# Kernel tuning notes

Hardware: AMD Instinct MI355X
Metric: run time of the kernel (lower is better)

The kernel has to match this reference:

```python
import jax, jax.numpy as jnp
import numpy as np

B, S, D = 4, 2048, 1024
NH, HD = 16, 64  # num_heads, head_dim; NH*HD == D


def setup_inputs() -> dict:
    key = jax.random.key(0)
    ks = jax.random.split(key, 10)
    s = 0.02
    return {
        "x": jax.random.normal(ks[0], (B, S, D), dtype=jnp.float32),
        "attention_mask": jnp.zeros((B, 1, 1, S), dtype=jnp.float32),
        "Wq": jax.random.normal(ks[1], (D, D), dtype=jnp.float32) * s,
        "bq": jnp.zeros((D,), dtype=jnp.float32),
        "Wk": jax.random.normal(ks[2], (D, D), dtype=jnp.float32) * s,
        "bk": jnp.zeros((D,), dtype=jnp.float32),
        "Wv": jax.random.normal(ks[3], (D, D), dtype=jnp.float32) * s,
        "bv": jnp.zeros((D,), dtype=jnp.float32),
        "Wo": jax.random.normal(ks[4], (D, D), dtype=jnp.float32) * s,
        "bo": jnp.zeros((D,), dtype=jnp.float32),
    }


def _heads(t):
    # [B,S,D] -> [B,NH,S,HD]
    return t.reshape(B, S, NH, HD).transpose(0, 2, 1, 3)


def reference(x, attention_mask, Wq, bq, Wk, bk, Wv, bv, Wo, bo):
    q = _heads(x @ Wq + bq)
    k = _heads(x @ Wk + bk)
    v = _heads(x @ Wv + bv)
    scores = jnp.einsum("bhqd,bhkd->bhqk", q, k) / jnp.sqrt(jnp.float32(HD))
    scores = scores + attention_mask
    attn = jax.nn.softmax(scores, axis=-1)  # dropout p=0 -> identity
    ctx = jnp.einsum("bhqk,bhkd->bhqd", attn, v)
    ctx = ctx.transpose(0, 2, 1, 3).reshape(B, S, D)
    return ctx @ Wo + bo
```

## Files before the change

kernel.cpp:

```cpp
#include <hip/hip_runtime.h>
#include <cstdint>
#include <cstddef>

typedef unsigned short u16;
typedef __attribute__((ext_vector_type(8))) __bf16 bf16x8;
typedef __attribute__((ext_vector_type(4))) float f32x4;
typedef __attribute__((ext_vector_type(16))) float f32x16;
typedef __attribute__((ext_vector_type(2))) uint32_t u32x2;
typedef __attribute__((ext_vector_type(4))) float float4v;

#define BATCH 4
#define S_LEN 2048
#define DMODEL 1024
#define NHEAD 16
#define HDIM 64
#define MROWS (BATCH * S_LEN)
#define LOG2E 1.4426950408889634f
#define SC_L (0.125f * LOG2E)

__device__ __forceinline__ u16 f2bf(float f) {
  uint32_t u = __float_as_uint(f);
  u += 0x7fffu + ((u >> 16) & 1u);
  return (u16)(u >> 16);
}

#if __has_builtin(__builtin_amdgcn_cvt_pk_bf16_f32)
__device__ __forceinline__ uint32_t packbf2(float a, float b) {
  auto t = __builtin_amdgcn_cvt_pk_bf16_f32(a, b);
  uint32_t u;
  __builtin_memcpy(&u, &t, 4);
  return u;
}
#else
__device__ __forceinline__ uint32_t packbf2(float a, float b) {
  uint32_t ua = __float_as_uint(a) + 0x8000u;
  uint32_t ub = __float_as_uint(b) + 0x8000u;
  return (ub & 0xFFFF0000u) | (ua >> 16);
}
#endif

#if __has_builtin(__builtin_amdgcn_exp2f)
#define EXP2(x) __builtin_amdgcn_exp2f(x)
#else
#define EXP2(x) exp2f(x)
#endif

typedef __attribute__((address_space(1))) void gvoid_t;
typedef __attribute__((address_space(3))) void svoid_t;
__device__ __forceinline__ void gl_lds16(const void* g, void* s) {
  __builtin_amdgcn_global_load_lds((gvoid_t*)g, (svoid_t*)s, 16, 0, 0);
}

#define NB_CVT (MROWS * DMODEL / 4 / 256)
#define NB_W   4096
__global__ __launch_bounds__(256) void prep_kernel(const float4v* __restrict__ x,
                                                   u32x2* __restrict__ xb,
                                                   const float* __restrict__ W0,
                                                   const float* __restrict__ W1,
                                                   const float* __restrict__ W2,
                                                   const float* __restrict__ W3,
                                                   u16* __restrict__ Wall,
                                                   const float* __restrict__ mask,
                                                   float* __restrict__ mL) {
  __shared__ float tile[32][33];
  const int bid = blockIdx.x;
  const int tid = threadIdx.x;
  if (bid < NB_CVT) {
    const int i = bid * 256 + tid;
    float4v v = x[i];
    u32x2 o;
    o.x = packbf2(v.x, v.y);
    o.y = packbf2(v.z, v.w);
    xb[i] = o;
    return;
  }
  if (bid >= NB_CVT + NB_W) {
    const int i = (bid - NB_CVT - NB_W) * 256 + tid;
    mL[i] = mask[i] * LOG2E;
    return;
  }
  const int r = bid - NB_CVT;
  const int z = r >> 10;
  const int rem = r & 1023;
  const float* W = (z == 0) ? W0 : (z == 1) ? W1 : (z == 2) ? W2 : W3;
  u16* Wt = Wall + (size_t)z * DMODEL * DMODEL;
  const int n0 = (rem & 31) * 32, k0 = (rem >> 5) * 32;
  const int xx = tid & 31, y = tid >> 5;
  for (int yy = y; yy < 32; yy += 8)
    tile[yy][xx] = W[(size_t)(k0 + yy) * DMODEL + n0 + xx];
  __syncthreads();
  for (int yy = y; yy < 32; yy += 8)
    Wt[(size_t)(n0 + yy) * DMODEL + k0 + xx] = f2bf(tile[xx][yy]);
}

template <int MODE>
__global__ __launch_bounds__(256) void gemm128(const u16* __restrict__ A,
                                               const u16* __restrict__ Bt,
                                               const float* __restrict__ b0,
                                               const float* __restrict__ b1,
                                               const float* __restrict__ b2,
                                               void* __restrict__ o0,
                                               void* __restrict__ o1,
                                               void* __restrict__ o2) {
  __shared__ u16 As[2 * 128 * 32];
  __shared__ u16 Bs[2 * 128 * 32];
  const int tid = threadIdx.x;
  const int wid = tid >> 6;
  const int lane = tid & 63;
  const int l16 = lane & 15;
  const int g4 = lane >> 4;
  const int m0 = blockIdx.x * 128;
  const int n0 = blockIdx.y * 128;
  const int wm = (wid & 1) * 64;
  const int wn = (wid >> 1) * 64;

  const int srow = tid >> 2;
  const int sk = (tid & 3) * 8;
  const u16* gA = A + (size_t)(m0 + srow) * DMODEL + sk;
  const u16* gB = Bt + (size_t)(n0 + srow) * DMODEL + sk;
  char* sA = (char*)As + wid * 1024;
  char* sB = (char*)Bs + wid * 1024;

  f32x4 acc[4][4];
#pragma unroll
  for (int i = 0; i < 4; ++i)
#pragma unroll
    for (int j = 0; j < 4; ++j) acc[i][j] = (f32x4){0.f, 0.f, 0.f, 0.f};

  for (int k0 = 0; k0 < DMODEL; k0 += 64) {
    __syncthreads();
    gl_lds16(gA + k0, sA);
    gl_lds16(gA + (size_t)64 * DMODEL + k0, sA + 4096);
    gl_lds16(gB + k0, sB);
    gl_lds16(gB + (size_t)64 * DMODEL + k0, sB + 4096);
    gl_lds16(gA + k0 + 32, sA + 8192);
    gl_lds16(gA + (size_t)64 * DMODEL + k0 + 32, sA + 12288);
    gl_lds16(gB + k0 + 32, sB + 8192);
    gl_lds16(gB + (size_t)64 * DMODEL + k0 + 32, sB + 12288);
    __syncthreads();

#pragma unroll
    for (int kk = 0; kk < 2; ++kk) {
      const u16* Ab = As + kk * 4096;
      const u16* Bb = Bs + kk * 4096;
      bf16x8 af[4], bfr[4];
#pragma unroll
      for (int i = 0; i < 4; ++i)
        af[i] = *(const bf16x8*)(Ab + (wm + i * 16 + l16) * 32 + g4 * 8);
#pragma unroll
      for (int j = 0; j < 4; ++j)
        bfr[j] = *(const bf16x8*)(Bb + (wn + j * 16 + l16) * 32 + g4 * 8);
#pragma unroll
      for (int i = 0; i < 4; ++i)
#pragma unroll
        for (int j = 0; j < 4; ++j)
          acc[i][j] = __builtin_amdgcn_mfma_f32_16x16x32_bf16(af[i], bfr[j],
                                                              acc[i][j], 0, 0, 0);
    }
  }

  const int seg = n0 >> 10;
  const float* bp = (MODE == 1 || seg == 0) ? b0 : (seg == 1 ? b1 : b2);
  void* op = (MODE == 1 || seg == 0) ? o0 : (seg == 1 ? o1 : o2);

#pragma unroll
  for (int i = 0; i < 4; ++i) {
#pragma unroll
    for (int j = 0; j < 4; ++j) {
      const int coll = n0 + wn + j * 16 + l16;
      const int cseg = coll & 1023;
      const float bval = bp[cseg];
#pragma unroll
      for (int r = 0; r < 4; ++r) {
        const int rowg = m0 + wm + i * 16 + g4 * 4 + r;
        const float v = acc[i][j][r] + bval;
        if (MODE == 0) {
          const int b = rowg >> 11, s = rowg & (S_LEN - 1);
          const int h = cseg >> 6, d = cseg & (HDIM - 1);
          if (seg == 2) {
            ((u16*)op)[(((size_t)(b * NHEAD + h) * HDIM + d) << 11) + s] = f2bf(v);
          } else {
            ((u16*)op)[((size_t)((b * NHEAD + h) * S_LEN + s) << 6) + d] = f2bf(v);
          }
        } else {
          ((float*)op)[(size_t)rowg * DMODEL + cseg] = v;
        }
      }
    }
  }
}

__global__ __launch_bounds__(256, 2) void attn8_kernel(const u16* __restrict__ Q,
                                                       const u16* __restrict__ K,
                                                       const u16* __restrict__ Vt,
                                                       const float* __restrict__ maskL,
                                                       u16* __restrict__ ctx) {
  __shared__ u16 Ks[64 * 72];
  __shared__ u16 Vs[64 * 72];

  const int tid = threadIdx.x;
  const int wid = tid >> 6;
  const int lane = tid & 63;
  const int l32 = lane & 31;
  const int hi = lane >> 5;
  const int flat = blockIdx.y * gridDim.x + blockIdx.x;
  const int nf = (flat & 7) * 64 + (flat >> 3);
  const int bx = nf & 7;
  const int bh = nf >> 3;
  const int b = bh >> 4;
  const int h = bh & 15;
  const int qw0 = bx * 256 + wid * 64;

  const u16* Qbase = Q + (size_t)bh * S_LEN * HDIM;
  bf16x8 aq[2][4];
#pragma unroll
  for (int qh = 0; qh < 2; ++qh)
#pragma unroll
    for (int c = 0; c < 4; ++c)
      aq[qh][c] = *(const bf16x8*)(Qbase + (size_t)(qw0 + qh * 32 + l32) * HDIM +
                                   c * 16 + hi * 8);

  const f32x16 z16 = {};
  f32x16 oacc[2][2] = {};
  float lsum[2] = {0.f, 0.f};

  const int srow = tid >> 3;
  const int scol = (tid & 7) * 8;
  const int keyg = scol >> 4;
  const int todd = (scol >> 3) & 1;
  const int vkb = keyg * 16 + todd * 4;
  const u16* Kg = K + (size_t)bh * S_LEN * HDIM + (size_t)srow * HDIM + scol;
  const u16* Vg = Vt + (size_t)bh * HDIM * S_LEN + (size_t)srow * S_LEN + scol;
  const float* mrow = maskL + (size_t)b * S_LEN;

  for (int kt = 0; kt < S_LEN; kt += 64) {
    bf16x8 kv0 = *(const bf16x8*)(Kg + (size_t)kt * HDIM);
    bf16x8 kv1 = *(const bf16x8*)(Kg + (size_t)(kt + 32) * HDIM);
    union { bf16x8 v; uint32_t u[4]; } vv0, vv1;
    vv0.v = *(const bf16x8*)(Vg + kt);
    vv1.v = *(const bf16x8*)(Vg + (size_t)32 * S_LEN + kt);
    __syncthreads();
    *(bf16x8*)(Ks + srow * 72 + scol) = kv0;
    *(bf16x8*)(Ks + (srow + 32) * 72 + scol) = kv1;
    *(u32x2*)(Vs + srow * 72 + vkb) = (u32x2){vv0.u[0], vv0.u[1]};
    *(u32x2*)(Vs + srow * 72 + vkb + 8) = (u32x2){vv0.u[2], vv0.u[3]};
    *(u32x2*)(Vs + (srow + 32) * 72 + vkb) = (u32x2){vv1.u[0], vv1.u[1]};
    *(u32x2*)(Vs + (srow + 32) * 72 + vkb + 8) = (u32x2){vv1.u[2], vv1.u[3]};
    __syncthreads();

    uint32_t P[2][2][8];
#pragma unroll
    for (int T = 0; T < 2; ++T) {
      bf16x8 kf[4];
#pragma unroll
      for (int c = 0; c < 4; ++c)
        kf[c] = *(const bf16x8*)(Ks + (T * 32 + l32) * 72 + c * 16 + hi * 8);
      f32x4 m4[4];
#pragma unroll
      for (int tq = 0; tq < 4; ++tq)
        m4[tq] = *(const f32x4*)(mrow + kt + T * 32 + tq * 8 + hi * 4);
#pragma unroll
      for (int qh = 0; qh < 2; ++qh) {
        f32x16 s = __builtin_amdgcn_mfma_f32_32x32x16_bf16(kf[0], aq[qh][0], z16, 0, 0, 0);
#pragma unroll
        for (int c = 1; c < 4; ++c)
          s = __builtin_amdgcn_mfma_f32_32x32x16_bf16(kf[c], aq[qh][c], s, 0, 0, 0);
        float lacc_t = 0.f;
#pragma unroll
        for (int tq = 0; tq < 4; ++tq) {
          float p0 = EXP2(fmaf(s[tq * 4 + 0], SC_L, m4[tq][0]));
          float p1 = EXP2(fmaf(s[tq * 4 + 1], SC_L, m4[tq][1]));
          float p2 = EXP2(fmaf(s[tq * 4 + 2], SC_L, m4[tq][2]));
          float p3 = EXP2(fmaf(s[tq * 4 + 3], SC_L, m4[tq][3]));
          P[T][qh][tq * 2] = packbf2(p0, p1);
          P[T][qh][tq * 2 + 1] = packbf2(p2, p3);
          lacc_t += (p0 + p1) + (p2 + p3);
        }
        lsum[qh] += lacc_t;
      }
    }

#pragma unroll
    for (int c = 0; c < 4; ++c) {
      const int T = c >> 1, half = c & 1;
      bf16x8 vf[2];
#pragma unroll
      for (int dh = 0; dh < 2; ++dh)
        vf[dh] = *(const bf16x8*)(Vs + (dh * 32 + l32) * 72 + c * 16 + hi * 8);
#pragma unroll
      for (int qh = 0; qh < 2; ++qh) {
        union { uint32_t u[4]; bf16x8 v; } pf;
#pragma unroll
        for (int e = 0; e < 4; ++e) pf.u[e] = P[T][qh][half * 4 + e];
        oacc[qh][0] = __builtin_amdgcn_mfma_f32_32x32x16_bf16(pf.v, vf[0], oacc[qh][0], 0, 0, 0);
        oacc[qh][1] = __builtin_amdgcn_mfma_f32_32x32x16_bf16(pf.v, vf[1], oacc[qh][1], 0, 0, 0);
      }
    }
  }

  float lt[2];
#pragma unroll
  for (int qh = 0; qh < 2; ++qh)
    lt[qh] = lsum[qh] + __shfl_xor(lsum[qh], 32);

#pragma unroll
  for (int qh = 0; qh < 2; ++qh) {
#pragma unroll
    for (int reg = 0; reg < 16; ++reg) {
      const int qloc = (reg & 3) + 8 * (reg >> 2) + 4 * hi;
      const int q = qw0 + qh * 32 + qloc;
      const float inv = 1.0f / __shfl(lt[qh], qloc);
      u16* cp = ctx + ((size_t)(b * S_LEN + q) * NHEAD + h) * HDIM;
      cp[l32] = f2bf(oacc[qh][0][reg] * inv);
      cp[32 + l32] = f2bf(oacc[qh][1][reg] * inv);
    }
  }
}

extern "C" void kernel_launch(void* const* d_in, const int* in_sizes, int n_in,
                              void* d_out, int out_size, void* d_ws, size_t ws_size,
                              hipStream_t stream) {
  const float* x = (const float*)d_in[0];
  const float* mask = (const float*)d_in[1];
  const float* Wq = (const float*)d_in[2];
  const float* bq = (const float*)d_in[3];
  const float* Wk = (const float*)d_in[4];
  const float* bk = (const float*)d_in[5];
  const float* Wv = (const float*)d_in[6];
  const float* bv = (const float*)d_in[7];
  const float* Wo = (const float*)d_in[8];
  const float* bo = (const float*)d_in[9];
  float* out = (float*)d_out;

  char* ws = (char*)d_ws;
  size_t off = 0;
  u16* xb = (u16*)(ws + off);    off += (size_t)MROWS * DMODEL * 2;
  u16* wall = (u16*)(ws + off);  off += (size_t)4 * DMODEL * DMODEL * 2;
  u16* Qh = (u16*)(ws + off);    off += (size_t)MROWS * DMODEL * 2;
  u16* Kh = (u16*)(ws + off);    off += (size_t)MROWS * DMODEL * 2;
  u16* Vtb = (u16*)(ws + off);   off += (size_t)MROWS * DMODEL * 2;
  u16* ctxb = (u16*)(ws + off);  off += (size_t)MROWS * DMODEL * 2;
  float* mL = (float*)(ws + off); off += (size_t)BATCH * S_LEN * 4;
  (void)ws_size; (void)in_sizes; (void)n_in; (void)out_size;

  prep_kernel<<<dim3(NB_CVT + NB_W + BATCH * S_LEN / 256), dim3(256), 0, stream>>>(
      (const float4v*)x, (u32x2*)xb, Wq, Wk, Wv, Wo, wall, mask, mL);

  gemm128<0><<<dim3(MROWS / 128, 3 * DMODEL / 128), dim3(256), 0, stream>>>(
      xb, wall, bq, bk, bv, (void*)Qh, (void*)Kh, (void*)Vtb);

  attn8_kernel<<<dim3(S_LEN / 256, BATCH * NHEAD), dim3(256), 0, stream>>>(Qh, Kh, Vtb, mL, ctxb);

  gemm128<1><<<dim3(MROWS / 128, DMODEL / 128), dim3(256), 0, stream>>>(
      ctxb, wall + (size_t)3 * DMODEL * DMODEL, bo, bo, bo, (void*)out, (void*)out, (void*)out);
}
```

Before: 289.4 us.

## Double attention key tile per barrier and compute row sums via MFMA with ones

The attention kernel now stages 128 keys per iteration instead of 64, so it does half as many syncthreads pairs and issues more global loads in flight. The softmax denominator is no longer summed with scalar adds and a cross-lane shuffle. It is accumulated by an extra MFMA of P against a ones vector, which leaves the sum already in the output register layout. This trades VALU adds and shuffles for extra matrix-core work (50% more PV MFMAs), plus higher LDS use and register pressure. The sum is now taken over the bf16-rounded P values.

```diff
diff --git a/kernel.cpp b/kernel.cpp
--- a/kernel.cpp
+++ b/kernel.cpp
@@ -190,13 +190,13 @@
   }
 }
 
-__global__ __launch_bounds__(256, 2) void attn8_kernel(const u16* __restrict__ Q,
+__global__ __launch_bounds__(256, 2) void attn9_kernel(const u16* __restrict__ Q,
                                                        const u16* __restrict__ K,
                                                        const u16* __restrict__ Vt,
                                                        const float* __restrict__ maskL,
                                                        u16* __restrict__ ctx) {
-  __shared__ u16 Ks[64 * 72];
-  __shared__ u16 Vs[64 * 72];
+  __shared__ u16 Ks[128 * 72];
+  __shared__ u16 Vs[64 * 136];
 
   const int tid = threadIdx.x;
   const int wid = tid >> 6;
@@ -220,9 +220,14 @@
       aq[qh][c] = *(const bf16x8*)(Qbase + (size_t)(qw0 + qh * 32 + l32) * HDIM +
                                    c * 16 + hi * 8);
 
+  union { u16 s[8]; bf16x8 v; } onesu;
+#pragma unroll
+  for (int i = 0; i < 8; ++i) onesu.s[i] = 0x3F80;
+  const bf16x8 onesv = onesu.v;
+
   const f32x16 z16 = {};
   f32x16 oacc[2][2] = {};
-  float lsum[2] = {0.f, 0.f};
+  f32x16 lacc[2] = {};
 
   const int srow = tid >> 3;
   const int scol = (tid & 7) * 8;
@@ -233,83 +238,92 @@
   const u16* Vg = Vt + (size_t)bh * HDIM * S_LEN + (size_t)srow * S_LEN + scol;
   const float* mrow = maskL + (size_t)b * S_LEN;
 
-  for (int kt = 0; kt < S_LEN; kt += 64) {
+  for (int kt = 0; kt < S_LEN; kt += 128) {
     bf16x8 kv0 = *(const bf16x8*)(Kg + (size_t)kt * HDIM);
     bf16x8 kv1 = *(const bf16x8*)(Kg + (size_t)(kt + 32) * HDIM);
-    union { bf16x8 v; uint32_t u[4]; } vv0, vv1;
+    bf16x8 kv2 = *(const bf16x8*)(Kg + (size_t)(kt + 64) * HDIM);
+    bf16x8 kv3 = *(const bf16x8*)(Kg + (size_t)(kt + 96) * HDIM);
+    union { bf16x8 v; uint32_t u[4]; } vv0, vv1, vv2, vv3;
     vv0.v = *(const bf16x8*)(Vg + kt);
     vv1.v = *(const bf16x8*)(Vg + (size_t)32 * S_LEN + kt);
+    vv2.v = *(const bf16x8*)(Vg + kt + 64);
+    vv3.v = *(const bf16x8*)(Vg + (size_t)32 * S_LEN + kt + 64);
     __syncthreads();
     *(bf16x8*)(Ks + srow * 72 + scol) = kv0;
     *(bf16x8*)(Ks + (srow + 32) * 72 + scol) = kv1;
-    *(u32x2*)(Vs + srow * 72 + vkb) = (u32x2){vv0.u[0], vv0.u[1]};
-    *(u32x2*)(Vs + srow * 72 + vkb + 8) = (u32x2){vv0.u[2], vv0.u[3]};
-    *(u32x2*)(Vs + (srow + 32) * 72 + vkb) = (u32x2){vv1.u[0], vv1.u[1]};
-    *(u32x2*)(Vs + (srow + 32) * 72 + vkb + 8) = (u32x2){vv1.u[2], vv1.u[3]};
+    *(bf16x8*)(Ks + (srow + 64) * 72 + scol) = kv2;
+    *(bf16x8*)(Ks + (srow + 96) * 72 + scol) = kv3;
+    *(u32x2*)(Vs + srow * 136 + vkb) = (u32x2){vv0.u[0], vv0.u[1]};
+    *(u32x2*)(Vs + srow * 136 + vkb + 8) = (u32x2){vv0.u[2], vv0.u[3]};
+    *(u32x2*)(Vs + (srow + 32) * 136 + vkb) = (u32x2){vv1.u[0], vv1.u[1]};
+    *(u32x2*)(Vs + (srow + 32) * 136 + vkb + 8) = (u32x2){vv1.u[2], vv1.u[3]};
+    *(u32x2*)(Vs + srow * 136 + 64 + vkb) = (u32x2){vv2.u[0], vv2.u[1]};
+    *(u32x2*)(Vs + srow * 136 + 64 + vkb + 8) = (u32x2){vv2.u[2], vv2.u[3]};
+    *(u32x2*)(Vs + (srow + 32) * 136 + 64 + vkb) = (u32x2){vv3.u[0], vv3.u[1]};
+    *(u32x2*)(Vs + (srow + 32) * 136 + 64 + vkb + 8) = (u32x2){vv3.u[2], vv3.u[3]};
     __syncthreads();
 
-    uint32_t P[2][2][8];
-#pragma unroll
-    for (int T = 0; T < 2; ++T) {
-      bf16x8 kf[4];
-#pragma unroll
-      for (int c = 0; c < 4; ++c)
-        kf[c] = *(const bf16x8*)(Ks + (T * 32 + l32) * 72 + c * 16 + hi * 8);
-      f32x4 m4[4];
-#pragma unroll
-      for (int tq = 0; tq < 4; ++tq)
-        m4[tq] = *(const f32x4*)(mrow + kt + T * 32 + tq * 8 + hi * 4);
-#pragma unroll
-      for (int qh = 0; qh < 2; ++qh) {
-        f32x16 s = __builtin_amdgcn_mfma_f32_32x32x16_bf16(kf[0], aq[qh][0], z16, 0, 0, 0);
-#pragma unroll
-        for (int c = 1; c < 4; ++c)
-          s = __builtin_amdgcn_mfma_f32_32x32x16_bf16(kf[c], aq[qh][c], s, 0, 0, 0);
-        float lacc_t = 0.f;
-#pragma unroll
-        for (int tq = 0; tq < 4; ++tq) {
-          float p0 = EXP2(fmaf(s[tq * 4 + 0], SC_L, m4[tq][0]));
-          float p1 = EXP2(fmaf(s[tq * 4 + 1], SC_L, m4[tq][1]));
-          float p2 = EXP2(fmaf(s[tq * 4 + 2], SC_L, m4[tq][2]));
-          float p3 = EXP2(fmaf(s[tq * 4 + 3], SC_L, m4[tq][3]));
-          P[T][qh][tq * 2] = packbf2(p0, p1);
-          P[T][qh][tq * 2 + 1] = packbf2(p2, p3);
-          lacc_t += (p0 + p1) + (p2 + p3);
+#pragma unroll
+    for (int ko = 0; ko < 128; ko += 64) {
+      const u16* Kb = Ks + ko * 72;
+      const u16* Vb = Vs + ko;
+      const float* mko = mrow + kt + ko;
+
+      uint32_t P[2][2][8];
+#pragma unroll
+      for (int T = 0; T < 2; ++T) {
+        bf16x8 kf[4];
+#pragma unroll
+        for (int c = 0; c < 4; ++c)
+          kf[c] = *(const bf16x8*)(Kb + (T * 32 + l32) * 72 + c * 16 + hi * 8);
+        f32x4 m4[4];
+#pragma unroll
+        for (int tq = 0; tq < 4; ++tq)
+          m4[tq] = *(const f32x4*)(mko + T * 32 + tq * 8 + hi * 4);
+#pragma unroll
+        for (int qh = 0; qh < 2; ++qh) {
+          f32x16 s = __builtin_amdgcn_mfma_f32_32x32x16_bf16(kf[0], aq[qh][0], z16, 0, 0, 0);
+#pragma unroll
+          for (int c = 1; c < 4; ++c)
+            s = __builtin_amdgcn_mfma_f32_32x32x16_bf16(kf[c], aq[qh][c], s, 0, 0, 0);
+#pragma unroll
+          for (int tq = 0; tq < 4; ++tq) {
+            float p0 = EXP2(fmaf(s[tq * 4 + 0], SC_L, m4[tq][0]));
+            float p1 = EXP2(fmaf(s[tq * 4 + 1], SC_L, m4[tq][1]));
+            float p2 = EXP2(fmaf(s[tq * 4 + 2], SC_L, m4[tq][2]));
+            float p3 = EXP2(fmaf(s[tq * 4 + 3], SC_L, m4[tq][3]));
+            P[T][qh][tq * 2] = packbf2(p0, p1);
+            P[T][qh][tq * 2 + 1] = packbf2(p2, p3);
+          }
         }
-        lsum[qh] += lacc_t;
+      }
+
+#pragma unroll
+      for (int c = 0; c < 4; ++c) {
+        const int T = c >> 1, half = c & 1;
+        bf16x8 vf[2];
+#pragma unroll
+        for (int dh = 0; dh < 2; ++dh)
+          vf[dh] = *(const bf16x8*)(Vb + (dh * 32 + l32) * 136 + c * 16 + hi * 8);
+#pragma unroll
+        for (int qh = 0; qh < 2; ++qh) {
+          union { uint32_t u[4]; bf16x8 v; } pf;
+#pragma unroll
+          for (int e = 0; e < 4; ++e) pf.u[e] = P[T][qh][half * 4 + e];
+          oacc[qh][0] = __builtin_amdgcn_mfma_f32_32x32x16_bf16(pf.v, vf[0], oacc[qh][0], 0, 0, 0);
+          oacc[qh][1] = __builtin_amdgcn_mfma_f32_32x32x16_bf16(pf.v, vf[1], oacc[qh][1], 0, 0, 0);
+          lacc[qh] = __builtin_amdgcn_mfma_f32_32x32x16_bf16(pf.v, onesv, lacc[qh], 0, 0, 0);
+        }
       }
     }
-
-#pragma unroll
-    for (int c = 0; c < 4; ++c) {
-      const int T = c >> 1, half = c & 1;
-      bf16x8 vf[2];
-#pragma unroll
-      for (int dh = 0; dh < 2; ++dh)
-        vf[dh] = *(const bf16x8*)(Vs + (dh * 32 + l32) * 72 + c * 16 + hi * 8);
-#pragma unroll
-      for (int qh = 0; qh < 2; ++qh) {
-        union { uint32_t u[4]; bf16x8 v; } pf;
-#pragma unroll
-        for (int e = 0; e < 4; ++e) pf.u[e] = P[T][qh][half * 4 + e];
-        oacc[qh][0] = __builtin_amdgcn_mfma_f32_32x32x16_bf16(pf.v, vf[0], oacc[qh][0], 0, 0, 0);
-        oacc[qh][1] = __builtin_amdgcn_mfma_f32_32x32x16_bf16(pf.v, vf[1], oacc[qh][1], 0, 0, 0);
-      }
-    }
-  }
-
-  float lt[2];
-#pragma unroll
-  for (int qh = 0; qh < 2; ++qh)
-    lt[qh] = lsum[qh] + __shfl_xor(lsum[qh], 32);
+  }
 
 #pragma unroll
   for (int qh = 0; qh < 2; ++qh) {
 #pragma unroll
     for (int reg = 0; reg < 16; ++reg) {
-      const int qloc = (reg & 3) + 8 * (reg >> 2) + 4 * hi;
-      const int q = qw0 + qh * 32 + qloc;
-      const float inv = 1.0f / __shfl(lt[qh], qloc);
+      const int q = qw0 + qh * 32 + (reg & 3) + 8 * (reg >> 2) + 4 * hi;
+      const float inv = 1.0f / lacc[qh][reg];
       u16* cp = ctx + ((size_t)(b * S_LEN + q) * NHEAD + h) * HDIM;
       cp[l32] = f2bf(oacc[qh][0][reg] * inv);
       cp[32 + l32] = f2bf(oacc[qh][1][reg] * inv);
@@ -349,7 +363,7 @@
   gemm128<0><<<dim3(MROWS / 128, 3 * DMODEL / 128), dim3(256), 0, stream>>>(
       xb, wall, bq, bk, bv, (void*)Qh, (void*)Kh, (void*)Vtb);
 
-  attn8_kernel<<<dim3(S_LEN / 256, BATCH * NHEAD), dim3(256), 0, stream>>>(Qh, Kh, Vtb, mL, ctxb);
+  attn9_kernel<<<dim3(S_LEN / 256, BATCH * NHEAD), dim3(256), 0, stream>>>(Qh, Kh, Vtb, mL, ctxb);
 
   gemm128<1><<<dim3(MROWS / 128, DMODEL / 128), dim3(256), 0, stream>>>(
       ctxb, wall + (size_t)3 * DMODEL * DMODEL, bo, bo, bo, (void*)out, (void*)out, (void*)out);
```

Result: no change. 290.0 us (+0.2%).

## Load K/V fragments directly from global and compute softmax row sums via MFMA

Applied to the files above, without the earlier changes.

The attention kernel stops staging K and V tiles through shared memory and drops both per-iteration __syncthreads; each wave now reads its MFMA operand fragments straight from global memory, relying on L1/L2 to serve the reuse across the block's four waves. The softmax denominator is no longer summed with scalar adds and a cross-lane shuffle. Instead an extra MFMA multiplies P by a ones vector, which leaves each row sum in the same register layout as the output accumulator. This trades LDS traffic and barriers for redundant global/cache loads, including narrower 8-byte V loads, plus extra MFMA work.

```diff
diff --git a/kernel.cpp b/kernel.cpp
--- a/kernel.cpp
+++ b/kernel.cpp
@@ -190,14 +190,11 @@
   }
 }
 
-__global__ __launch_bounds__(256, 2) void attn8_kernel(const u16* __restrict__ Q,
-                                                       const u16* __restrict__ K,
-                                                       const u16* __restrict__ Vt,
-                                                       const float* __restrict__ maskL,
-                                                       u16* __restrict__ ctx) {
-  __shared__ u16 Ks[64 * 72];
-  __shared__ u16 Vs[64 * 72];
-
+__global__ __launch_bounds__(256, 2) void attn10_kernel(const u16* __restrict__ Q,
+                                                        const u16* __restrict__ K,
+                                                        const u16* __restrict__ Vt,
+                                                        const float* __restrict__ maskL,
+                                                        u16* __restrict__ ctx) {
   const int tid = threadIdx.x;
   const int wid = tid >> 6;
   const int lane = tid & 63;
@@ -220,41 +217,29 @@
       aq[qh][c] = *(const bf16x8*)(Qbase + (size_t)(qw0 + qh * 32 + l32) * HDIM +
                                    c * 16 + hi * 8);
 
+  union { u16 s[8]; bf16x8 v; } onesu;
+#pragma unroll
+  for (int i = 0; i < 8; ++i) onesu.s[i] = 0x3F80;
+  const bf16x8 onesv = onesu.v;
+
   const f32x16 z16 = {};
   f32x16 oacc[2][2] = {};
-  float lsum[2] = {0.f, 0.f};
-
-  const int srow = tid >> 3;
-  const int scol = (tid & 7) * 8;
-  const int keyg = scol >> 4;
-  const int todd = (scol >> 3) & 1;
-  const int vkb = keyg * 16 + todd * 4;
-  const u16* Kg = K + (size_t)bh * S_LEN * HDIM + (size_t)srow * HDIM + scol;
-  const u16* Vg = Vt + (size_t)bh * HDIM * S_LEN + (size_t)srow * S_LEN + scol;
+  f32x16 lacc[2] = {};
+
+  const u16* Kf = K + (size_t)bh * S_LEN * HDIM + (size_t)l32 * HDIM + hi * 8;
+  const u16* Vb = Vt + (size_t)bh * HDIM * S_LEN;
+  const u16* Vf0 = Vb + (size_t)l32 * S_LEN + hi * 4;
+  const u16* Vf1 = Vb + (size_t)(32 + l32) * S_LEN + hi * 4;
   const float* mrow = maskL + (size_t)b * S_LEN;
 
   for (int kt = 0; kt < S_LEN; kt += 64) {
-    bf16x8 kv0 = *(const bf16x8*)(Kg + (size_t)kt * HDIM);
-    bf16x8 kv1 = *(const bf16x8*)(Kg + (size_t)(kt + 32) * HDIM);
-    union { bf16x8 v; uint32_t u[4]; } vv0, vv1;
-    vv0.v = *(const bf16x8*)(Vg + kt);
-    vv1.v = *(const bf16x8*)(Vg + (size_t)32 * S_LEN + kt);
-    __syncthreads();
-    *(bf16x8*)(Ks + srow * 72 + scol) = kv0;
-    *(bf16x8*)(Ks + (srow + 32) * 72 + scol) = kv1;
-    *(u32x2*)(Vs + srow * 72 + vkb) = (u32x2){vv0.u[0], vv0.u[1]};
-    *(u32x2*)(Vs + srow * 72 + vkb + 8) = (u32x2){vv0.u[2], vv0.u[3]};
-    *(u32x2*)(Vs + (srow + 32) * 72 + vkb) = (u32x2){vv1.u[0], vv1.u[1]};
-    *(u32x2*)(Vs + (srow + 32) * 72 + vkb + 8) = (u32x2){vv1.u[2], vv1.u[3]};
-    __syncthreads();
-
     uint32_t P[2][2][8];
 #pragma unroll
     for (int T = 0; T < 2; ++T) {
       bf16x8 kf[4];
 #pragma unroll
       for (int c = 0; c < 4; ++c)
-        kf[c] = *(const bf16x8*)(Ks + (T * 32 + l32) * 72 + c * 16 + hi * 8);
+        kf[c] = *(const bf16x8*)(Kf + (size_t)(kt + T * 32) * HDIM + c * 16);
       f32x4 m4[4];
 #pragma unroll
       for (int tq = 0; tq < 4; ++tq)
@@ -265,7 +250,6 @@
 #pragma unroll
         for (int c = 1; c < 4; ++c)
           s = __builtin_amdgcn_mfma_f32_32x32x16_bf16(kf[c], aq[qh][c], s, 0, 0, 0);
-        float lacc_t = 0.f;
 #pragma unroll
         for (int tq = 0; tq < 4; ++tq) {
           float p0 = EXP2(fmaf(s[tq * 4 + 0], SC_L, m4[tq][0]));
@@ -274,9 +258,7 @@
           float p3 = EXP2(fmaf(s[tq * 4 + 3], SC_L, m4[tq][3]));
           P[T][qh][tq * 2] = packbf2(p0, p1);
           P[T][qh][tq * 2 + 1] = packbf2(p2, p3);
-          lacc_t += (p0 + p1) + (p2 + p3);
         }
-        lsum[qh] += lacc_t;
       }
     }
 
@@ -285,8 +267,13 @@
       const int T = c >> 1, half = c & 1;
       bf16x8 vf[2];
 #pragma unroll
-      for (int dh = 0; dh < 2; ++dh)
-        vf[dh] = *(const bf16x8*)(Vs + (dh * 32 + l32) * 72 + c * 16 + hi * 8);
+      for (int dh = 0; dh < 2; ++dh) {
+        const u16* vp = (dh ? Vf1 : Vf0) + kt + c * 16;
+        union { uint64_t q[2]; bf16x8 v; } vu;
+        vu.q[0] = *(const uint64_t*)(vp);
+        vu.q[1] = *(const uint64_t*)(vp + 8);
+        vf[dh] = vu.v;
+      }
 #pragma unroll
       for (int qh = 0; qh < 2; ++qh) {
         union { uint32_t u[4]; bf16x8 v; } pf;
@@ -294,22 +281,17 @@
         for (int e = 0; e < 4; ++e) pf.u[e] = P[T][qh][half * 4 + e];
         oacc[qh][0] = __builtin_amdgcn_mfma_f32_32x32x16_bf16(pf.v, vf[0], oacc[qh][0], 0, 0, 0);
         oacc[qh][1] = __builtin_amdgcn_mfma_f32_32x32x16_bf16(pf.v, vf[1], oacc[qh][1], 0, 0, 0);
+        lacc[qh] = __builtin_amdgcn_mfma_f32_32x32x16_bf16(pf.v, onesv, lacc[qh], 0, 0, 0);
       }
     }
   }
 
-  float lt[2];
-#pragma unroll
-  for (int qh = 0; qh < 2; ++qh)
-    lt[qh] = lsum[qh] + __shfl_xor(lsum[qh], 32);
-
 #pragma unroll
   for (int qh = 0; qh < 2; ++qh) {
 #pragma unroll
     for (int reg = 0; reg < 16; ++reg) {
-      const int qloc = (reg & 3) + 8 * (reg >> 2) + 4 * hi;
-      const int q = qw0 + qh * 32 + qloc;
-      const float inv = 1.0f / __shfl(lt[qh], qloc);
+      const int q = qw0 + qh * 32 + (reg & 3) + 8 * (reg >> 2) + 4 * hi;
+      const float inv = 1.0f / lacc[qh][reg];
       u16* cp = ctx + ((size_t)(b * S_LEN + q) * NHEAD + h) * HDIM;
       cp[l32] = f2bf(oacc[qh][0][reg] * inv);
       cp[32 + l32] = f2bf(oacc[qh][1][reg] * inv);
@@ -349,7 +331,7 @@
   gemm128<0><<<dim3(MROWS / 128, 3 * DMODEL / 128), dim3(256), 0, stream>>>(
       xb, wall, bq, bk, bv, (void*)Qh, (void*)Kh, (void*)Vtb);
 
-  attn8_kernel<<<dim3(S_LEN / 256, BATCH * NHEAD), dim3(256), 0, stream>>>(Qh, Kh, Vtb, mL, ctxb);
+  attn10_kernel<<<dim3(S_LEN / 256, BATCH * NHEAD), dim3(256), 0, stream>>>(Qh, Kh, Vtb, mL, ctxb);
 
   gemm128<1><<<dim3(MROWS / 128, DMODEL / 128), dim3(256), 0, stream>>>(
       ctxb, wall + (size_t)3 * DMODEL * DMODEL, bo, bo, bo, (void*)out, (void*)out, (void*)out);
```

Result: slower. 396.2 us (+36.9%).
